# Kernel optimization log

Hardware: AMD Instinct MI355X
Metric: run time of the kernel (lower is better)

Reference implementation:

```python
import jax, jax.numpy as jnp
import numpy as np

DECAY = 0.99
EPS = 1e-05


def setup_inputs() -> dict:
    key = jax.random.key(0)
    k1, k2, k3 = jax.random.split(key, 3)
    return {
        "input": jax.random.normal(k1, (32, 64, 64, 64), dtype=jnp.float32),
        "embed": jax.random.normal(k2, (64, 512), dtype=jnp.float32),
        "cluster_size": jnp.zeros((512,), dtype=jnp.float32),
        "embed_avg": jax.random.normal(k3, (64, 512), dtype=jnp.float32),
    }


def reference(input, embed, cluster_size, embed_avg):
    n_embed = embed.shape[1]
    flatten = input.reshape(-1, input.shape[-1])  # [N, dim]
    dist = (
        jnp.sum(flatten * flatten, axis=1, keepdims=True)
        - 2.0 * flatten @ embed
        + jnp.sum(embed * embed, axis=0, keepdims=True)
    )  # [N, n_embed]
    embed_ind_flat = jnp.argmin(dist, axis=1)  # [N]
    embed_ind = embed_ind_flat.reshape(input.shape[:-1])
    quantize = jnp.take(embed.T, embed_ind_flat, axis=0).reshape(input.shape)
    diff = jnp.mean((quantize - input) ** 2)

    # EMA codebook update (training path; buffer updates returned as outputs)
    embed_onehot_sum = jnp.zeros((n_embed,), dtype=flatten.dtype).at[embed_ind_flat].add(1.0)
    embed_sum = jax.ops.segment_sum(flatten, embed_ind_flat, num_segments=n_embed).T  # [dim, n_embed]
    new_cluster_size = cluster_size * DECAY + (1.0 - DECAY) * embed_onehot_sum
    new_embed_avg = embed_avg * DECAY + (1.0 - DECAY) * embed_sum
    n = jnp.sum(new_cluster_size)
    cs = (new_cluster_size + EPS) / (n + n_embed * EPS) * n
    new_embed = new_embed_avg / cs[None, :]

    # straight-through estimator
    quantize_st = input + jax.lax.stop_gradient(quantize - input)
    return (quantize_st, diff, embed_ind, new_embed, new_cluster_size, new_embed_avg)
```

## Files before the change

kernel.cpp:

```cpp
#include <hip/hip_runtime.h>

#define DIM     64
#define N_EMBED 512
#define N_ROWS  131072
#define XPAD    129
#define TPITCH  513

__global__ void prep_kernel(const float* __restrict__ embed,
                            float* __restrict__ se,
                            float* __restrict__ embed_t,
                            int do_et) {
    int j = blockIdx.x * blockDim.x + threadIdx.x;
    if (j >= N_EMBED) return;
    float s = 0.f;
#pragma unroll
    for (int d = 0; d < DIM; d += 4) {
        float b0 = embed[(d + 0) * N_EMBED + j];
        float b1 = embed[(d + 1) * N_EMBED + j];
        float b2 = embed[(d + 2) * N_EMBED + j];
        float b3 = embed[(d + 3) * N_EMBED + j];
        s = fmaf(b0, b0, s); s = fmaf(b1, b1, s);
        s = fmaf(b2, b2, s); s = fmaf(b3, b3, s);
        if (do_et) {
            float4 v; v.x = b0; v.y = b1; v.z = b2; v.w = b3;
            *reinterpret_cast<float4*>(&embed_t[j * DIM + d]) = v;
        }
    }
    se[j] = s;
}

__launch_bounds__(256, 2)
__global__ void vq_assign(const float* __restrict__ input,
                          const float* __restrict__ embed,
                          const float* __restrict__ se,
                          float* __restrict__ out_ind,
                          int*   __restrict__ ind) {
    __shared__ float Xs[64][XPAD];
    __shared__ float Es[64][XPAD];
    __shared__ float sxs[128];

    const int t    = threadIdx.x;
    const int row0 = blockIdx.x * 128;
    const int tr   = t >> 4;
    const int tc   = t & 15;
    const int bx   = ((tc >> 2) & 1) * 4;

#pragma unroll
    for (int ph = 0; ph < 8; ++ph) {
        int idx = ph * 256 + t;
        int row = idx >> 4;
        int kq  = idx & 15;
        float4 v = *reinterpret_cast<const float4*>(
            &input[(size_t)(row0 + row) * 64 + kq * 4]);
        Xs[kq * 4 + 0][row] = v.x;
        Xs[kq * 4 + 1][row] = v.y;
        Xs[kq * 4 + 2][row] = v.z;
        Xs[kq * 4 + 3][row] = v.w;
    }
    __syncthreads();

    if (t < 128) {
        float s = 0.f;
#pragma unroll 8
        for (int k = 0; k < 64; ++k) { float x = Xs[k][t]; s = fmaf(x, x, s); }
        sxs[t] = s;
    }

    float bestd[8], sx[8];
    int   bestj[8];
#pragma unroll
    for (int r = 0; r < 8; ++r) { bestd[r] = INFINITY; bestj[r] = 0; }

    for (int chunk = 0; chunk < 4; ++chunk) {
        const int ccb = chunk * 128;
        __syncthreads();
#pragma unroll
        for (int ph = 0; ph < 8; ++ph) {
            int idx = ph * 256 + t;
            int k   = idx >> 5;
            int cq  = idx & 31;
            float4 v = *reinterpret_cast<const float4*>(
                &embed[k * N_EMBED + ccb + cq * 4]);
            *reinterpret_cast<float4*>(&Es[k][(cq * 4) ^ (((cq >> 3) & 1) * 4)]) = v;
        }
        __syncthreads();
        if (chunk == 0) {
#pragma unroll
            for (int r = 0; r < 8; ++r) sx[r] = sxs[tr * 8 + r];
        }

        float acc[8][8];
#pragma unroll
        for (int r = 0; r < 8; ++r)
#pragma unroll
            for (int c = 0; c < 8; ++c) acc[r][c] = 0.f;

#pragma unroll 2
        for (int k = 0; k < 64; ++k) {
            float a[8], b[8];
            *reinterpret_cast<float4*>(&a[0]) = *reinterpret_cast<const float4*>(&Xs[k][tr * 8]);
            *reinterpret_cast<float4*>(&a[4]) = *reinterpret_cast<const float4*>(&Xs[k][tr * 8 + 4]);
            *reinterpret_cast<float4*>(&b[0]) = *reinterpret_cast<const float4*>(&Es[k][(tc * 8) ^ bx]);
            *reinterpret_cast<float4*>(&b[4]) = *reinterpret_cast<const float4*>(&Es[k][(tc * 8 + 4) ^ bx]);
#pragma unroll
            for (int r = 0; r < 8; ++r)
#pragma unroll
                for (int c = 0; c < 8; ++c)
                    acc[r][c] = fmaf(a[r], b[c], acc[r][c]);
        }

#pragma unroll
        for (int c = 0; c < 8; ++c) {
            int j = ccb + tc * 8 + c;
            float sej = se[j];
#pragma unroll
            for (int r = 0; r < 8; ++r) {
                float d = (sx[r] - 2.f * acc[r][c]) + sej;
                if (d < bestd[r]) { bestd[r] = d; bestj[r] = j; }
            }
        }
    }

    __syncthreads();
    float* rd = &Es[0][0];
    int*   rj = (int*)(rd + 128 * 17);
#pragma unroll
    for (int r = 0; r < 8; ++r) {
        rd[(tr * 8 + r) * 17 + tc] = bestd[r];
        rj[(tr * 8 + r) * 17 + tc] = bestj[r];
    }
    __syncthreads();
    if (t < 128) {
        float bd = rd[t * 17 + 0];
        int   bj = rj[t * 17 + 0];
#pragma unroll
        for (int w = 1; w < 16; ++w) {
            float dw = rd[t * 17 + w];
            int   jw = rj[t * 17 + w];
            if (dw < bd || (dw == bd && jw < bj)) { bd = dw; bj = jw; }
        }
        out_ind[row0 + t] = (float)bj;
        ind[row0 + t]     = bj;
    }
}

__launch_bounds__(512, 1)
__global__ void vq_post2(const float* __restrict__ input,
                         const float* __restrict__ embed,
                         const float* __restrict__ embed_t,
                         const int* __restrict__ ind,
                         float* __restrict__ out_q,
                         float* __restrict__ esum,
                         float* __restrict__ counts,
                         double* __restrict__ diff_acc,
                         int have_et) {
    __shared__ float tab[DIM * TPITCH];
    __shared__ float lcount[N_EMBED];
    __shared__ float wsum[8];
    const int t    = threadIdx.x;
    const int wave = t >> 6;
    const int lane = t & 63;

    for (int i = t; i < DIM * TPITCH; i += 512) tab[i] = 0.f;
    lcount[t] = 0.f;
    __syncthreads();

    const int rbase = blockIdx.x * 512 + wave * 64;
    float dsum = 0.f;

#pragma unroll 4
    for (int it = 0; it < 64; ++it) {
        const int row = rbase + it;
        const int j = ind[row];
        const float x = input[(size_t)row * DIM + lane];
        float e;
        if (have_et) e = embed_t[j * DIM + lane];
        else         e = embed[lane * N_EMBED + j];
        const float d0 = e - x;
        out_q[(size_t)row * DIM + lane] = x + d0;
        dsum = fmaf(d0, d0, dsum);
        atomicAdd(&tab[lane * TPITCH + j], x);
        if (lane == 0) atomicAdd(&lcount[j], 1.0f);
    }
    __syncthreads();

    for (int i = t; i < DIM * N_EMBED; i += 512) {
        const int d = i >> 9, j = i & 511;
        float v = tab[d * TPITCH + j];
        if (v != 0.f) atomicAdd(&esum[i], v);
    }
    {
        float v = lcount[t];
        if (v != 0.f) atomicAdd(&counts[t], v);
    }

    for (int off = 32; off > 0; off >>= 1) dsum += __shfl_down(dsum, off, 64);
    if (lane == 0) wsum[wave] = dsum;
    __syncthreads();
    if (t == 0) {
        float b = 0.f;
#pragma unroll
        for (int w = 0; w < 8; ++w) b += wsum[w];
        atomicAdd(diff_acc, (double)b);
    }
}

__global__ void fin_a(const float* __restrict__ cluster_size,
                      const float* __restrict__ counts,
                      float* __restrict__ out_ncs,
                      float* __restrict__ nstore) {
    int t = threadIdx.x;
    float ncs = cluster_size[t] * 0.99f + 0.01f * counts[t];
    out_ncs[t] = ncs;
    __shared__ float red[512];
    red[t] = ncs;
    __syncthreads();
    for (int s = 256; s > 0; s >>= 1) {
        if (t < s) red[t] += red[t + s];
        __syncthreads();
    }
    if (t == 0) nstore[0] = red[0];
}

__global__ void fin_b(const float* __restrict__ embed_avg,
                      const float* __restrict__ esum,
                      const float* __restrict__ out_ncs,
                      const float* __restrict__ nstore,
                      const double* __restrict__ diff_acc,
                      float* __restrict__ out_ne,
                      float* __restrict__ out_nea,
                      float* __restrict__ out_diff) {
    int e = blockIdx.x * 512 + threadIdx.x;
    const float EPSF = 1e-5f;
    float n = nstore[0];
    int j = e & (N_EMBED - 1);
    float ncs = out_ncs[j];
    float cs = (ncs + EPSF) / (n + 512.0f * EPSF) * n;
    float es = embed_avg[e] * 0.99f + 0.01f * esum[e];
    out_nea[e] = es;
    out_ne[e] = es / cs;
    if (e == 0) out_diff[0] = (float)(*diff_acc * (1.0 / 8388608.0));
}

extern "C" void kernel_launch(void* const* d_in, const int* in_sizes, int n_in,
                              void* d_out, int out_size, void* d_ws, size_t ws_size,
                              hipStream_t stream) {
    const float* input        = (const float*)d_in[0];
    const float* embed        = (const float*)d_in[1];
    const float* cluster_size = (const float*)d_in[2];
    const float* embed_avg    = (const float*)d_in[3];

    float* out_q    = (float*)d_out;
    float* out_diff = out_q + 8388608;
    float* out_ind  = out_diff + 1;
    float* out_ne   = out_ind + 131072;
    float* out_ncs  = out_ne + 32768;
    float* out_nea  = out_ncs + 512;

    char*   ws       = (char*)d_ws;
    double* diff_acc = (double*)ws;
    float*  nstore   = (float*)(ws + 64);
    float*  counts   = (float*)(ws + 256);
    float*  se       = (float*)(ws + 4096);
    int*    ind      = (int*)(ws + 8192);
    float*  esum     = (float*)(ws + 8192 + 524288);
    float*  embed_t  = (float*)(ws + 8192 + 524288 + 131072);

    const size_t need_et = 8192 + 524288 + 131072 + 131072;
    const int have_et = (ws_size >= need_et) ? 1 : 0;

    hipMemsetAsync(ws, 0, 4096, stream);
    hipMemsetAsync(ws + 8192 + 524288, 0, 131072, stream);

    prep_kernel<<<2, 256, 0, stream>>>(embed, se, embed_t, have_et);
    vq_assign<<<1024, 256, 0, stream>>>(input, embed, se, out_ind, ind);
    vq_post2<<<256, 512, 0, stream>>>(input, embed, embed_t, ind, out_q, esum,
                                      counts, diff_acc, have_et);
    fin_a<<<1, 512, 0, stream>>>(cluster_size, counts, out_ncs, nstore);
    fin_b<<<64, 512, 0, stream>>>(embed_avg, esum, out_ncs, nstore, diff_acc,
                                  out_ne, out_nea, out_diff);
}
```

Measured before the change: 290.1 us.

## Fuse quantize output and diff into assign kernel; split esum into dim-grouped kernel

Moves the quantized-output write and squared-error accumulation into the assignment kernel, where the chosen code index is already in shared memory and the input tile was just read. The embed-sum scatter moves to a new kernel that splits dimensions into 8 groups with a small per-block shared table, giving 512 blocks instead of 256 and much less shared memory per block. Counts become integer atomics. XPAD changes from 129 to 132, which may alter bank conflicts in the assign tile. The new kernel still reads the input a second time, and the assign kernel gains extra global traffic and a tail.

```diff
diff --git a/kernel.cpp b/kernel.cpp
--- a/kernel.cpp
+++ b/kernel.cpp
@@ -3,8 +3,7 @@
 #define DIM     64
 #define N_EMBED 512
 #define N_ROWS  131072
-#define XPAD    129
-#define TPITCH  513
+#define XPAD    132
 
 __global__ void prep_kernel(const float* __restrict__ embed,
                             float* __restrict__ se,
@@ -33,11 +32,17 @@
 __global__ void vq_assign(const float* __restrict__ input,
                           const float* __restrict__ embed,
                           const float* __restrict__ se,
+                          const float* __restrict__ embed_t,
                           float* __restrict__ out_ind,
-                          int*   __restrict__ ind) {
+                          int*   __restrict__ ind,
+                          float* __restrict__ out_q,
+                          double* __restrict__ diff_acc,
+                          int have_et) {
     __shared__ float Xs[64][XPAD];
     __shared__ float Es[64][XPAD];
     __shared__ float sxs[128];
+    __shared__ int   bjs[128];
+    __shared__ float wsum2[4];
 
     const int t    = threadIdx.x;
     const int row0 = blockIdx.x * 128;
@@ -141,76 +146,103 @@
         }
         out_ind[row0 + t] = (float)bj;
         ind[row0 + t]     = bj;
-    }
-}
-
-__launch_bounds__(512, 1)
-__global__ void vq_post2(const float* __restrict__ input,
-                         const float* __restrict__ embed,
-                         const float* __restrict__ embed_t,
-                         const int* __restrict__ ind,
-                         float* __restrict__ out_q,
-                         float* __restrict__ esum,
-                         float* __restrict__ counts,
-                         double* __restrict__ diff_acc,
-                         int have_et) {
-    __shared__ float tab[DIM * TPITCH];
-    __shared__ float lcount[N_EMBED];
-    __shared__ float wsum[8];
+        bjs[t]            = bj;
+    }
+    __syncthreads();
+
+    const int erow  = t >> 1;
+    const int ehalf = t & 1;
+    const int grow  = row0 + erow;
+    const int bj2   = bjs[erow];
+    const float* xr = input + (size_t)grow * DIM + ehalf * 32;
+    float*       oq = out_q + (size_t)grow * DIM + ehalf * 32;
+    float dsum = 0.f;
+
+    if (have_et) {
+        const float* er = embed_t + (size_t)bj2 * DIM + ehalf * 32;
+#pragma unroll
+        for (int i = 0; i < 32; i += 4) {
+            float4 xv = *reinterpret_cast<const float4*>(xr + i);
+            float4 ev = *reinterpret_cast<const float4*>(er + i);
+            float t0 = ev.x - xv.x, t1 = ev.y - xv.y;
+            float t2 = ev.z - xv.z, t3 = ev.w - xv.w;
+            float4 o;
+            o.x = xv.x + t0; o.y = xv.y + t1; o.z = xv.z + t2; o.w = xv.w + t3;
+            *reinterpret_cast<float4*>(oq + i) = o;
+            dsum = fmaf(t0, t0, dsum); dsum = fmaf(t1, t1, dsum);
+            dsum = fmaf(t2, t2, dsum); dsum = fmaf(t3, t3, dsum);
+        }
+    } else {
+#pragma unroll
+        for (int i = 0; i < 32; ++i) {
+            float x = xr[i];
+            float e = embed[(ehalf * 32 + i) * N_EMBED + bj2];
+            float t0 = e - x;
+            oq[i] = x + t0;
+            dsum = fmaf(t0, t0, dsum);
+        }
+    }
+
+    for (int off = 32; off > 0; off >>= 1) dsum += __shfl_down(dsum, off, 64);
+    int lane = t & 63, wid = t >> 6;
+    if (lane == 0) wsum2[wid] = dsum;
+    __syncthreads();
+    if (t == 0) {
+        float b = wsum2[0] + wsum2[1] + wsum2[2] + wsum2[3];
+        atomicAdd(diff_acc, (double)b);
+    }
+}
+
+__launch_bounds__(256, 4)
+__global__ void vq_esum(const float* __restrict__ input,
+                        const int* __restrict__ ind,
+                        float* __restrict__ esum,
+                        int* __restrict__ gcount) {
+    const int dimg = blockIdx.x & 7;
+    const int rowg = blockIdx.x >> 3;
     const int t    = threadIdx.x;
-    const int wave = t >> 6;
+    const int w    = t >> 6;
     const int lane = t & 63;
-
-    for (int i = t; i < DIM * TPITCH; i += 512) tab[i] = 0.f;
-    lcount[t] = 0.f;
-    __syncthreads();
-
-    const int rbase = blockIdx.x * 512 + wave * 64;
-    float dsum = 0.f;
+    const int rloc = lane >> 3;
+    const int d    = lane & 7;
+
+    __shared__ float tab[8][513];
+    __shared__ int   lcnt[N_EMBED];
+
+    for (int i = t; i < 8 * 513; i += 256) (&tab[0][0])[i] = 0.f;
+    if (dimg == 0) { lcnt[t] = 0; lcnt[t + 256] = 0; }
+    __syncthreads();
+
+    const int rbase = rowg * 2048;
+    const int dbase = dimg * 8;
 
 #pragma unroll 4
     for (int it = 0; it < 64; ++it) {
-        const int row = rbase + it;
+        const int row = rbase + it * 32 + w * 8 + rloc;
         const int j = ind[row];
-        const float x = input[(size_t)row * DIM + lane];
-        float e;
-        if (have_et) e = embed_t[j * DIM + lane];
-        else         e = embed[lane * N_EMBED + j];
-        const float d0 = e - x;
-        out_q[(size_t)row * DIM + lane] = x + d0;
-        dsum = fmaf(d0, d0, dsum);
-        atomicAdd(&tab[lane * TPITCH + j], x);
-        if (lane == 0) atomicAdd(&lcount[j], 1.0f);
-    }
-    __syncthreads();
-
-    for (int i = t; i < DIM * N_EMBED; i += 512) {
-        const int d = i >> 9, j = i & 511;
-        float v = tab[d * TPITCH + j];
-        if (v != 0.f) atomicAdd(&esum[i], v);
-    }
-    {
-        float v = lcount[t];
-        if (v != 0.f) atomicAdd(&counts[t], v);
-    }
-
-    for (int off = 32; off > 0; off >>= 1) dsum += __shfl_down(dsum, off, 64);
-    if (lane == 0) wsum[wave] = dsum;
-    __syncthreads();
-    if (t == 0) {
-        float b = 0.f;
-#pragma unroll
-        for (int w = 0; w < 8; ++w) b += wsum[w];
-        atomicAdd(diff_acc, (double)b);
+        const float x = input[(size_t)row * DIM + dbase + d];
+        atomicAdd(&tab[d][j], x);
+        if (dimg == 0 && d == 0) atomicAdd(&lcnt[j], 1);
+    }
+    __syncthreads();
+
+    for (int i = t; i < 8 * N_EMBED; i += 256) {
+        const int dl = i >> 9, j = i & 511;
+        float v = tab[dl][j];
+        if (v != 0.f) atomicAdd(&esum[(dbase + dl) * N_EMBED + j], v);
+    }
+    if (dimg == 0) {
+        int v0 = lcnt[t];       if (v0) atomicAdd(&gcount[t], v0);
+        int v1 = lcnt[t + 256]; if (v1) atomicAdd(&gcount[t + 256], v1);
     }
 }
 
 __global__ void fin_a(const float* __restrict__ cluster_size,
-                      const float* __restrict__ counts,
+                      const int* __restrict__ gcount,
                       float* __restrict__ out_ncs,
                       float* __restrict__ nstore) {
     int t = threadIdx.x;
-    float ncs = cluster_size[t] * 0.99f + 0.01f * counts[t];
+    float ncs = cluster_size[t] * 0.99f + 0.01f * (float)gcount[t];
     out_ncs[t] = ncs;
     __shared__ float red[512];
     red[t] = ncs;
@@ -260,7 +292,7 @@
     char*   ws       = (char*)d_ws;
     double* diff_acc = (double*)ws;
     float*  nstore   = (float*)(ws + 64);
-    float*  counts   = (float*)(ws + 256);
+    int*    gcount   = (int*)(ws + 256);
     float*  se       = (float*)(ws + 4096);
     int*    ind      = (int*)(ws + 8192);
     float*  esum     = (float*)(ws + 8192 + 524288);
@@ -273,10 +305,10 @@
     hipMemsetAsync(ws + 8192 + 524288, 0, 131072, stream);
 
     prep_kernel<<<2, 256, 0, stream>>>(embed, se, embed_t, have_et);
-    vq_assign<<<1024, 256, 0, stream>>>(input, embed, se, out_ind, ind);
-    vq_post2<<<256, 512, 0, stream>>>(input, embed, embed_t, ind, out_q, esum,
-                                      counts, diff_acc, have_et);
-    fin_a<<<1, 512, 0, stream>>>(cluster_size, counts, out_ncs, nstore);
+    vq_assign<<<1024, 256, 0, stream>>>(input, embed, se, embed_t, out_ind, ind,
+                                        out_q, diff_acc, have_et);
+    vq_esum<<<512, 256, 0, stream>>>(input, ind, esum, gcount);
+    fin_a<<<1, 512, 0, stream>>>(cluster_size, gcount, out_ncs, nstore);
     fin_b<<<64, 512, 0, stream>>>(embed_avg, esum, out_ncs, nstore, diff_acc,
                                   out_ne, out_nea, out_diff);
 }
```

New measurement: 262.5 us. 9.5% less time.
